# Optimization experiments

Measured on AMD Instinct MI355X. Metric: run time of the kernel, lower is better.

Reference implementation:

```python
import jax, jax.numpy as jnp
import numpy as np

B, S, D, H = 2, 2048, 1024, 16
DK = D // H
ROPE_BASE = 10000


def _rope_tables(seq_len, dim):
    # RotaryEmbedding.__call__: freqs [S, dim/2], emb = concat([freqs, freqs]) -> [S, dim]
    inv_freq = 1.0 / (ROPE_BASE ** (jnp.arange(0, dim, 2, dtype=jnp.float32) / dim))
    t = jnp.arange(seq_len, dtype=jnp.float32)
    freqs = jnp.outer(t, inv_freq)
    emb = jnp.concatenate([freqs, freqs], axis=-1)
    return jnp.cos(emb), jnp.sin(emb)


def _apply_rope(x, cos, sin):
    # Faithful to apply_rotary_pos_emb: interleaved even/odd channel rotation
    cos = cos[None, None, :, :]  # [1,1,S,DK]
    sin = sin[None, None, :, :]
    x1 = x[..., 0::2]
    x2 = x[..., 1::2]
    r1 = x1 * cos[..., 0::2] - x2 * sin[..., 1::2]
    r2 = x1 * sin[..., 0::2] + x2 * cos[..., 1::2]
    return jnp.stack([r1, r2], axis=-1).reshape(x.shape)


def setup_inputs() -> dict:
    key = jax.random.key(0)
    ks = jax.random.split(key, 11)
    xavier = lambda k: jax.random.uniform(k, (D, D), jnp.float32,
                                          -jnp.sqrt(6.0 / (D + D)), jnp.sqrt(6.0 / (D + D)))
    return {
        "query": jax.random.normal(ks[0], (B, S, D), jnp.float32),
        "key": jax.random.normal(ks[1], (B, S, D), jnp.float32),
        "value": jax.random.normal(ks[2], (B, S, D), jnp.float32),
        "Wq": xavier(ks[3]), "bq": jnp.zeros((D,), jnp.float32),
        "Wk": xavier(ks[4]), "bk": jnp.zeros((D,), jnp.float32),
        "Wv": xavier(ks[5]), "bv": jnp.zeros((D,), jnp.float32),
        "Wo": xavier(ks[6]), "bo": jnp.zeros((D,), jnp.float32),
    }


def reference(query, key, value, Wq, bq, Wk, bk, Wv, bv, Wo, bo):
    def split_heads(x):  # [B,S,D] -> [B,H,S,DK]
        return x.reshape(B, S, H, DK).transpose(0, 2, 1, 3)

    q = split_heads(query @ Wq + bq)
    k = split_heads(key @ Wk + bk)
    v = split_heads(value @ Wv + bv)

    cos, sin = _rope_tables(S, DK)
    q = _apply_rope(q, cos, sin)
    k = _apply_rope(k, cos, sin)

    scores = jnp.einsum("bhqd,bhkd->bhqk", q, k) / jnp.sqrt(jnp.float32(DK))
    causal = jnp.tril(jnp.ones((S, S), dtype=bool))
    scores = jnp.where(causal, scores, jnp.float32(-1e10))
    attn = jax.nn.softmax(scores, axis=-1)
    out = jnp.einsum("bhqk,bhkd->bhqd", attn, v)  # [B,H,S,DK]
    out = out.transpose(0, 2, 1, 3).reshape(B, S, D)
    return out @ Wo + bo
```

## Files before the change

### kernel.cpp

```cpp
#include <hip/hip_runtime.h>
#include <hip/hip_bf16.h>
#include <math.h>

#define B_ 2
#define S_ 2048
#define D_ 1024
#define H_ 16
#define DK_ 64

#define ROPE_C 0.4152410118609203f
#define LOG2E 1.4426950408889634f

typedef float f4 __attribute__((ext_vector_type(4)));
typedef short s8 __attribute__((ext_vector_type(8)));

__device__ __forceinline__ ushort f2b(float f) {
  union { float f; uint u; } v; v.f = f;
  uint u = v.u + 0x7fffu + ((v.u >> 16) & 1u);
  return (ushort)(u >> 16);
}

__device__ __forceinline__ float b2f(ushort u) {
  union { uint u; float f; } v; v.u = ((uint)u) << 16;
  return v.f;
}

__device__ __forceinline__ uint cvtpk(float a, float b) {
  uint r;
  asm("v_cvt_pk_bf16_f32 %0, %1, %2" : "=v"(r) : "v"(a), "v"(b));
  return r;
}

__device__ __forceinline__ void async16(const ushort* g, ushort* l) {
  __builtin_amdgcn_global_load_lds(
      (const __attribute__((address_space(1))) uint*)g,
      (__attribute__((address_space(3))) uint*)l, 16, 0, 0);
}

__global__ __launch_bounds__(256) void prep_all(
    const float* __restrict__ q_in, const float* __restrict__ k_in,
    const float* __restrict__ v_in,
    ushort* __restrict__ Xbq, ushort* __restrict__ Xbk, ushort* __restrict__ Xbv,
    const float* __restrict__ Wq, const float* __restrict__ Wk,
    const float* __restrict__ Wv, const float* __restrict__ Wo,
    ushort* __restrict__ Wtqkv, ushort* __restrict__ Wto) {
  __shared__ ushort T[64][65];
  const int bid = blockIdx.x, t = threadIdx.x;
  if (bid < 6144) {
    const int m = bid >> 11;
    const float* in = (m == 0) ? q_in : (m == 1) ? k_in : v_in;
    ushort* out = (m == 0) ? Xbq : (m == 1) ? Xbk : Xbv;
    int idx = ((bid & 2047) * 256 + t) * 8;
    float4 a = *(const float4*)&in[idx];
    float4 b = *(const float4*)&in[idx + 4];
    ushort tmp[8] = {f2b(a.x), f2b(a.y), f2b(a.z), f2b(a.w),
                     f2b(b.x), f2b(b.y), f2b(b.z), f2b(b.w)};
    *(uint4*)&out[idx] = *(uint4*)tmp;
  } else {
    const int tb = bid - 6144;
    const int m = tb >> 8;
    const float* W = (m == 0) ? Wq : (m == 1) ? Wk : (m == 2) ? Wv : Wo;
    ushort* Wt = (m == 3) ? Wto : Wtqkv + (size_t)m * 1024 * 1024;
    const int k0 = (tb & 15) * 64, n0 = ((tb >> 4) & 15) * 64;
    #pragma unroll
    for (int i = 0; i < 16; ++i) {
      int e = t + i * 256, r = e >> 6, c = e & 63;
      T[c][r] = f2b(W[(size_t)(k0 + r) * D_ + n0 + c]);
    }
    __syncthreads();
    #pragma unroll
    for (int i = 0; i < 16; ++i) {
      int e = t + i * 256, r = e >> 6, c = e & 63;
      Wt[(size_t)(n0 + r) * D_ + k0 + c] = T[r][c];
    }
  }
}

template <int MODE>
__global__ __launch_bounds__(256) void gemm_mfma(
    const ushort* __restrict__ A0, const ushort* __restrict__ A1,
    const ushort* __restrict__ A2, const ushort* __restrict__ Bt,
    const float* __restrict__ bb0, const float* __restrict__ bb1,
    const float* __restrict__ bb2,
    ushort* __restrict__ oq, ushort* __restrict__ ok, ushort* __restrict__ ov,
    float* __restrict__ oo) {
  __shared__ ushort SM[16384];
  ushort* Es = SM;

  const int t = threadIdx.x, w = t >> 6, l = t & 63;
  const int m0 = blockIdx.x * 128, n0 = blockIdx.y * 128;
  const int wm = (w >> 1) * 64, wn = (w & 1) * 64;
  const int lm = l & 15, q4 = (l >> 4) * 4;
  const int hb = l >> 4;

  const ushort* A;
  const float* bias;
  int mat = 0;
  if constexpr (MODE == 0) {
    mat = n0 >> 10;
    A = (mat == 0) ? A0 : (mat == 1) ? A1 : A2;
    bias = (mat == 0) ? bb0 : (mat == 1) ? bb1 : bb2;
  } else {
    A = A0; bias = bb0;
  }

  const int srow = w * 32 + (l >> 2);
  const int pb = l & 3;
  const int lb = pb ^ (srow & 3);
  const ushort* gA = A + (size_t)(m0 + srow) * D_ + lb * 8;
  const ushort* gB = Bt + (size_t)(n0 + srow) * D_ + lb * 8;

#define GSTAGE(bf, kk)                                   \
  {                                                      \
    ushort* lA = SM + (bf) * 4096 + w * 1024;            \
    ushort* lB = SM + 8192 + (bf) * 4096 + w * 1024;     \
    async16(gA + (kk), lA);                              \
    async16(gA + 16 * D_ + (kk), lA + 512);              \
    async16(gB + (kk), lB);                              \
    async16(gB + 16 * D_ + (kk), lB + 512);              \
  }

  f4 acc[4][4];
  #pragma unroll
  for (int i = 0; i < 4; ++i)
    #pragma unroll
    for (int j = 0; j < 4; ++j) acc[i][j] = (f4){0.f, 0.f, 0.f, 0.f};

  GSTAGE(0, 0);
  __syncthreads();

  for (int k0 = 0; k0 < D_; k0 += 32) {
    const int bf = (k0 >> 5) & 1;
    if (k0 + 32 < D_) GSTAGE(bf ^ 1, k0 + 32);
    const ushort* Asb = SM + bf * 4096;
    const ushort* Bsb = SM + 8192 + bf * 4096;
    s8 af[4], bfr[4];
    #pragma unroll
    for (int mt = 0; mt < 4; ++mt) {
      int ra = wm + mt * 16 + lm;
      af[mt] = *(const s8*)&Asb[ra * 32 + ((hb ^ (ra & 3)) << 3)];
    }
    #pragma unroll
    for (int nt = 0; nt < 4; ++nt) {
      int rb = wn + nt * 16 + lm;
      bfr[nt] = *(const s8*)&Bsb[rb * 32 + ((hb ^ (rb & 3)) << 3)];
    }
    __builtin_amdgcn_s_setprio(1);
    #pragma unroll
    for (int mt = 0; mt < 4; ++mt)
      #pragma unroll
      for (int nt = 0; nt < 4; ++nt)
        acc[mt][nt] = __builtin_amdgcn_mfma_f32_16x16x32_bf16(af[mt], bfr[nt], acc[mt][nt], 0, 0, 0);
    __builtin_amdgcn_s_setprio(0);
    __syncthreads();
  }

  if constexpr (MODE == 2) {
    #pragma unroll
    for (int nt = 0; nt < 4; ++nt) {
      int n = n0 + wn + nt * 16 + lm;
      float bv = bias[n];
      #pragma unroll
      for (int mt = 0; mt < 4; ++mt)
        #pragma unroll
        for (int r = 0; r < 4; ++r)
          oo[(size_t)(m0 + wm + mt * 16 + q4 + r) * D_ + n] = acc[mt][nt][r] + bv;
    }
  } else {
    ushort* dst = (mat == 0) ? oq : (mat == 1) ? ok : ov;
    const int nm0 = n0 & 1023;
    #pragma unroll
    for (int p = 0; p < 2; ++p) {
      if ((w >> 1) == p) {
        #pragma unroll
        for (int nt = 0; nt < 4; ++nt) {
          int col = wn + nt * 16 + lm;
          float bv = bias[nm0 + col];
          #pragma unroll
          for (int mt = 0; mt < 4; ++mt)
            #pragma unroll
            for (int r = 0; r < 4; ++r)
              Es[(mt * 16 + q4 + r) * 144 + col] = f2b(acc[mt][nt][r] + bv);
        }
      }
      __syncthreads();
      #pragma unroll
      for (int i = 0; i < 4; ++i) {
        int e = t + i * 256, row = e >> 4, ch = e & 15;
        *(uint4*)&dst[(size_t)(m0 + p * 64 + row) * D_ + nm0 + ch * 8] =
            *(const uint4*)&Es[row * 144 + ch * 8];
      }
      __syncthreads();
    }
  }
#undef GSTAGE
}

__global__ __launch_bounds__(256) void rope_pass(
    const ushort* __restrict__ qtmp, const ushort* __restrict__ ktmp,
    const ushort* __restrict__ vtmp,
    ushort* __restrict__ qfb, ushort* __restrict__ kfb,
    ushort* __restrict__ vtb) {
  __shared__ ushort T[64][72];
  const int t = threadIdx.x;
  const int bh = blockIdx.x, st = blockIdx.y;
  const int b = bh >> 4, h = bh & 15;
  const int s0 = st * 64;
  const int r = t >> 2, c0 = (t & 3) * 16;
  const int s = s0 + r;

  float cs[16], sn[16];
  const float pos = (float)s;
  #pragma unroll
  for (int j = 0; j < 16; ++j) {
    float invf = exp2f(-(float)((c0 + j) & 31) * ROPE_C);
    __sincosf(pos * invf, &sn[j], &cs[j]);
  }

  const size_t src = ((size_t)(b * S_ + s)) * D_ + h * 64 + c0;
  const size_t dstqk = ((size_t)bh * S_ + s) * DK_ + c0;

  #pragma unroll
  for (int tensor = 0; tensor < 2; ++tensor) {
    const ushort* in = tensor ? ktmp : qtmp;
    ushort* out = tensor ? kfb : qfb;
    const float scale = tensor ? 1.f : 0.18033688011112042f;
    uint4 raw0 = *(const uint4*)&in[src];
    uint4 raw1 = *(const uint4*)&in[src + 8];
    ushort xr[16];
    *(uint4*)&xr[0] = raw0;
    *(uint4*)&xr[8] = raw1;
    float x[16];
    #pragma unroll
    for (int j = 0; j < 16; ++j) x[j] = b2f(xr[j]);
    ushort o[16];
    #pragma unroll
    for (int j = 0; j < 16; j += 2) {
      float e = x[j] * cs[j] - x[j + 1] * sn[j + 1];
      float d = x[j] * sn[j] + x[j + 1] * cs[j + 1];
      o[j] = f2b(e * scale);
      o[j + 1] = f2b(d * scale);
    }
    *(uint4*)&out[dstqk] = *(const uint4*)&o[0];
    *(uint4*)&out[dstqk + 8] = *(const uint4*)&o[8];
  }

  {
    uint4 raw0 = *(const uint4*)&vtmp[src];
    uint4 raw1 = *(const uint4*)&vtmp[src + 8];
    ushort xr[16];
    *(uint4*)&xr[0] = raw0;
    *(uint4*)&xr[8] = raw1;
    #pragma unroll
    for (int j = 0; j < 16; ++j) T[c0 + j][r] = xr[j];
    __syncthreads();
    const size_t dstv = ((size_t)bh * DK_ + r) * S_ + s0 + c0;
    *(uint4*)&vtb[dstv] = *(const uint4*)&T[r][c0];
    *(uint4*)&vtb[dstv + 8] = *(const uint4*)&T[r][c0 + 8];
  }
}

__global__ __launch_bounds__(256, 4) void attn_mfma(const ushort* __restrict__ qf,
                                                    const ushort* __restrict__ kf,
                                                    const ushort* __restrict__ vtf,
                                                    ushort* __restrict__ ctx) {
  __shared__ ushort Ks[2][4096];
  __shared__ ushort Vs[2][4096];
  __shared__ ushort PsS[4096];

  const int t = threadIdx.x, w = t >> 6, l = t & 63;
  const int bh = blockIdx.x, qt = 31 - (int)blockIdx.y;
  const int i0 = qt * 64;
  const int lm = l & 15, hb = l >> 4, h8 = hb * 8, q4 = hb * 4, w16 = w * 16;
  const size_t base = (size_t)bh * S_ * DK_;
  const int b = bh >> 4, h = bh & 15;

  const int sr = l >> 3, pbk = l & 7;
  const int rA = w * 16 + sr, rB = rA + 8;
  const int swS = (pbk ^ sr) << 3;
  const ushort* gkA = kf + base + (size_t)rA * DK_ + swS;
  const ushort* gkB = kf + base + (size_t)rB * DK_ + swS;
  const ushort* gvA = vtf + base + (size_t)rA * S_ + swS;
  const ushort* gvB = vtf + base + (size_t)rB * S_ + swS;

#define STAGE(bf, j0)                                       \
  {                                                         \
    ushort* lk = &Ks[bf][w * 1024];                         \
    ushort* lv = &Vs[bf][w * 1024];                         \
    async16(gkA + (size_t)(j0) * DK_, lk);                  \
    async16(gkB + (size_t)(j0) * DK_, lk + 512);            \
    async16(gvA + (j0), lv);                                \
    async16(gvB + (j0), lv + 512);                          \
  }

  const ushort* qp = qf + base + (size_t)(i0 + w16 + lm) * DK_ + h8;
  const s8 bq0 = *(const s8*)qp;
  const s8 bq1 = *(const s8*)(qp + 32);

  const int swr = lm & 7;
  const int cA = (hb ^ swr) << 3;
  const int cB = ((hb + 4) ^ swr) << 3;
  const int prow = (w16 + lm) * 64;
  const int psub = ((hb & 1) << 2) + ((hb >> 1) ^ swr);

  STAGE(0, 0);

  f4 O[4];
  #pragma unroll
  for (int i = 0; i < 4; ++i) O[i] = (f4){0.f, 0.f, 0.f, 0.f};
  float m_ = -1e30f, l_ = 0.f;

  __syncthreads();

  for (int jt = 0; jt <= qt; ++jt) {
    const int cur = jt & 1;
    if (jt < qt) STAGE(cur ^ 1, (jt + 1) * 64);
    const ushort* Kb = Ks[cur];
    const ushort* Vb = Vs[cur];

    f4 st[4];
    __builtin_amdgcn_s_setprio(1);
    #pragma unroll
    for (int nt = 0; nt < 4; ++nt) {
      const ushort* kRow = Kb + (nt * 16 + lm) * 64;
      s8 a0 = *(const s8*)&kRow[cA];
      s8 a1 = *(const s8*)&kRow[cB];
      f4 a = (f4){0.f, 0.f, 0.f, 0.f};
      a = __builtin_amdgcn_mfma_f32_16x16x32_bf16(a0, bq0, a, 0, 0, 0);
      a = __builtin_amdgcn_mfma_f32_16x16x32_bf16(a1, bq1, a, 0, 0, 0);
      st[nt] = a;
    }
    __builtin_amdgcn_s_setprio(0);

    if (jt == qt) {
      #pragma unroll
      for (int nt = 0; nt < 4; ++nt)
        #pragma unroll
        for (int r = 0; r < 4; ++r)
          if (nt * 16 + q4 + r > w16 + lm) st[nt][r] = -1e30f;
    }

    float x0 = fmaxf(fmaxf(st[0][0], st[0][1]), fmaxf(st[0][2], st[0][3]));
    float x1 = fmaxf(fmaxf(st[1][0], st[1][1]), fmaxf(st[1][2], st[1][3]));
    float x2 = fmaxf(fmaxf(st[2][0], st[2][1]), fmaxf(st[2][2], st[2][3]));
    float x3 = fmaxf(fmaxf(st[3][0], st[3][1]), fmaxf(st[3][2], st[3][3]));
    float pm = fmaxf(fmaxf(x0, x1), fmaxf(x2, x3));
    pm = fmaxf(pm, __shfl_xor(pm, 16));
    pm = fmaxf(pm, __shfl_xor(pm, 32));

    const bool stable = __all(pm <= m_ + 4.0f);
    float mn = m_, alpha = 1.f;
    if (!stable) {
      mn = fmaxf(m_, pm);
      alpha = exp2f(m_ - mn);
      m_ = mn;
    }

    #pragma unroll
    for (int nt = 0; nt < 4; ++nt)
      #pragma unroll
      for (int r = 0; r < 4; ++r)
        st[nt][r] = exp2f(st[nt][r] - mn);
    float s0 = (st[0][0] + st[0][1]) + (st[0][2] + st[0][3]);
    float s1 = (st[1][0] + st[1][1]) + (st[1][2] + st[1][3]);
    float s2 = (st[2][0] + st[2][1]) + (st[2][2] + st[2][3]);
    float s3 = (st[3][0] + st[3][1]) + (st[3][2] + st[3][3]);
    float ps = (s0 + s1) + (s2 + s3);
    ps += __shfl_xor(ps, 16);
    ps += __shfl_xor(ps, 32);

    if (stable) {
      l_ += ps;
    } else {
      l_ = l_ * alpha + ps;
      float ar[4];
      #pragma unroll
      for (int r = 0; r < 4; ++r) ar[r] = __shfl(alpha, q4 + r);
      #pragma unroll
      for (int nt = 0; nt < 4; ++nt)
        #pragma unroll
        for (int r = 0; r < 4; ++r) O[nt][r] *= ar[r];
    }

    #pragma unroll
    for (int nt = 0; nt < 4; ++nt) {
      uint2 pp;
      pp.x = cvtpk(st[nt][0], st[nt][1]);
      pp.y = cvtpk(st[nt][2], st[nt][3]);
      const int pidx = prow + ((((nt << 1) + (hb >> 1)) ^ swr) << 3) + ((hb & 1) << 2);
      *(uint2*)&PsS[pidx] = pp;
    }
    s8 ap0 = *(const s8*)&PsS[prow + cA];
    s8 ap1 = *(const s8*)&PsS[prow + cB];

    __builtin_amdgcn_s_setprio(1);
    #pragma unroll
    for (int nt = 0; nt < 4; ++nt) {
      const ushort* vRow = Vb + (nt * 16 + lm) * 64;
      s8 v0 = *(const s8*)&vRow[cA];
      s8 v1 = *(const s8*)&vRow[cB];
      O[nt] = __builtin_amdgcn_mfma_f32_16x16x32_bf16(ap0, v0, O[nt], 0, 0, 0);
      O[nt] = __builtin_amdgcn_mfma_f32_16x16x32_bf16(ap1, v1, O[nt], 0, 0, 0);
    }
    __builtin_amdgcn_s_setprio(0);

    __syncthreads();
  }

  float il[4];
  #pragma unroll
  for (int r = 0; r < 4; ++r) il[r] = 1.f / __shfl(l_, q4 + r);
  #pragma unroll
  for (int nt = 0; nt < 4; ++nt)
    #pragma unroll
    for (int r = 0; r < 4; ++r) {
      int row = w16 + q4 + r, col = nt * 16 + lm;
      PsS[row * 64 + ((((col >> 3) ^ (row & 7)) << 3)) + (col & 7)] =
          f2b(O[nt][r] * il[r]);
    }
  __syncthreads();
  #pragma unroll
  for (int i = 0; i < 2; ++i) {
    int e = t + i * 256, row = e >> 3, ch = e & 7;
    int s = i0 + row;
    *(uint4*)&ctx[((size_t)(b * S_ + s)) * D_ + h * 64 + ch * 8] =
        *(const uint4*)&PsS[row * 64 + ((ch ^ (row & 7)) << 3)];
  }
#undef STAGE
}

extern "C" void kernel_launch(void* const* d_in, const int* in_sizes, int n_in,
                              void* d_out, int out_size, void* d_ws, size_t ws_size,
                              hipStream_t stream) {
  const float* q_in = (const float*)d_in[0];
  const float* k_in = (const float*)d_in[1];
  const float* v_in = (const float*)d_in[2];
  const float* Wq = (const float*)d_in[3];
  const float* bq = (const float*)d_in[4];
  const float* Wk = (const float*)d_in[5];
  const float* bk = (const float*)d_in[6];
  const float* Wv = (const float*)d_in[7];
  const float* bv = (const float*)d_in[8];
  const float* Wo = (const float*)d_in[9];
  const float* bo = (const float*)d_in[10];

  const size_t NE = (size_t)B_ * S_ * D_;
  ushort* Xbq = (ushort*)d_ws;
  ushort* Xbk = Xbq + NE;
  ushort* Xbv = Xbk + NE;
  ushort* Wtqkv = Xbv + NE;
  ushort* Wto = Wtqkv + 3 * 1024 * 1024;
  ushort* qtmp = Wto + 1024 * 1024;
  ushort* ktmp = qtmp + NE;
  ushort* vtmp = ktmp + NE;
  ushort* qfb = vtmp + NE;
  ushort* kfb = qfb + NE;
  ushort* vtb = kfb + NE;
  ushort* ctxb = qtmp;

  prep_all<<<7168, 256, 0, stream>>>(q_in, k_in, v_in, Xbq, Xbk, Xbv,
                                     Wq, Wk, Wv, Wo, Wtqkv, Wto);

  gemm_mfma<0><<<dim3(32, 24), 256, 0, stream>>>(
      Xbq, Xbk, Xbv, Wtqkv, bq, bk, bv, qtmp, ktmp, vtmp, nullptr);

  rope_pass<<<dim3(32, 32), 256, 0, stream>>>(qtmp, ktmp, vtmp, qfb, kfb, vtb);

  attn_mfma<<<dim3(32, 32), 256, 0, stream>>>(qfb, kfb, vtb, ctxb);

  gemm_mfma<2><<<dim3(32, 8), 256, 0, stream>>>(
      ctxb, ctxb, ctxb, Wto, bo, bo, bo, nullptr, nullptr, nullptr,
      (float*)d_out);
}
```

Baseline: 228.7 us.

## Switch attention to 32x32x16 MFMA with two waves and register-shuffled P

After: 238.6 us. 1.04x slower.

```diff
diff --git a/kernel.cpp b/kernel.cpp
--- a/kernel.cpp
+++ b/kernel.cpp
@@ -12,6 +12,7 @@
 #define LOG2E 1.4426950408889634f
 
 typedef float f4 __attribute__((ext_vector_type(4)));
+typedef float f16x __attribute__((ext_vector_type(16)));
 typedef short s8 __attribute__((ext_vector_type(8)));
 
 __device__ __forceinline__ ushort f2b(float f) {
@@ -260,54 +261,49 @@
   }
 }
 
-__global__ __launch_bounds__(256, 4) void attn_mfma(const ushort* __restrict__ qf,
+__global__ __launch_bounds__(128, 2) void attn_mfma(const ushort* __restrict__ qf,
                                                     const ushort* __restrict__ kf,
                                                     const ushort* __restrict__ vtf,
                                                     ushort* __restrict__ ctx) {
   __shared__ ushort Ks[2][4096];
   __shared__ ushort Vs[2][4096];
-  __shared__ ushort PsS[4096];
 
   const int t = threadIdx.x, w = t >> 6, l = t & 63;
   const int bh = blockIdx.x, qt = 31 - (int)blockIdx.y;
   const int i0 = qt * 64;
-  const int lm = l & 15, hb = l >> 4, h8 = hb * 8, q4 = hb * 4, w16 = w * 16;
+  const int lo = l & 31, hi = l >> 5;
   const size_t base = (size_t)bh * S_ * DK_;
   const int b = bh >> 4, h = bh & 15;
 
   const int sr = l >> 3, pbk = l & 7;
-  const int rA = w * 16 + sr, rB = rA + 8;
   const int swS = (pbk ^ sr) << 3;
-  const ushort* gkA = kf + base + (size_t)rA * DK_ + swS;
-  const ushort* gkB = kf + base + (size_t)rB * DK_ + swS;
-  const ushort* gvA = vtf + base + (size_t)rA * S_ + swS;
-  const ushort* gvB = vtf + base + (size_t)rB * S_ + swS;
-
-#define STAGE(bf, j0)                                       \
-  {                                                         \
-    ushort* lk = &Ks[bf][w * 1024];                         \
-    ushort* lv = &Vs[bf][w * 1024];                         \
-    async16(gkA + (size_t)(j0) * DK_, lk);                  \
-    async16(gkB + (size_t)(j0) * DK_, lk + 512);            \
-    async16(gvA + (j0), lv);                                \
-    async16(gvB + (j0), lv + 512);                          \
-  }
-
-  const ushort* qp = qf + base + (size_t)(i0 + w16 + lm) * DK_ + h8;
-  const s8 bq0 = *(const s8*)qp;
-  const s8 bq1 = *(const s8*)(qp + 32);
-
-  const int swr = lm & 7;
-  const int cA = (hb ^ swr) << 3;
-  const int cB = ((hb + 4) ^ swr) << 3;
-  const int prow = (w16 + lm) * 64;
-  const int psub = ((hb & 1) << 2) + ((hb >> 1) ^ swr);
+  const ushort* gk = kf + base + (size_t)sr * DK_ + swS;
+  const ushort* gv = vtf + base + (size_t)sr * S_ + swS;
+
+#define STAGE(bf, j0)                                                      \
+  if (w == 0) {                                                            \
+    _Pragma("unroll")                                                      \
+    for (int i = 0; i < 8; ++i)                                            \
+      async16(gk + (size_t)((j0) + 8 * i) * DK_, &Ks[bf][i * 512]);        \
+  } else {                                                                 \
+    _Pragma("unroll")                                                      \
+    for (int i = 0; i < 8; ++i)                                            \
+      async16(gv + (size_t)(8 * i) * S_ + (j0), &Vs[bf][i * 512]);         \
+  }
+
+  const ushort* qp = qf + base + (size_t)(i0 + w * 32 + lo) * DK_;
+  s8 bq[4];
+  #pragma unroll
+  for (int s = 0; s < 4; ++s) bq[s] = *(const s8*)&qp[s * 16 + hi * 8];
+
+  const int rsw = lo & 7;
+  const int roff = lo * 64;
 
   STAGE(0, 0);
 
-  f4 O[4];
+  f16x O0, O1;
   #pragma unroll
-  for (int i = 0; i < 4; ++i) O[i] = (f4){0.f, 0.f, 0.f, 0.f};
+  for (int r = 0; r < 16; ++r) { O0[r] = 0.f; O1[r] = 0.f; }
   float m_ = -1e30f, l_ = 0.f;
 
   __syncthreads();
@@ -318,113 +314,128 @@
     const ushort* Kb = Ks[cur];
     const ushort* Vb = Vs[cur];
 
-    f4 st[4];
+    f16x s0, s1;
+    #pragma unroll
+    for (int r = 0; r < 16; ++r) { s0[r] = 0.f; s1[r] = 0.f; }
     __builtin_amdgcn_s_setprio(1);
     #pragma unroll
-    for (int nt = 0; nt < 4; ++nt) {
-      const ushort* kRow = Kb + (nt * 16 + lm) * 64;
-      s8 a0 = *(const s8*)&kRow[cA];
-      s8 a1 = *(const s8*)&kRow[cB];
-      f4 a = (f4){0.f, 0.f, 0.f, 0.f};
-      a = __builtin_amdgcn_mfma_f32_16x16x32_bf16(a0, bq0, a, 0, 0, 0);
-      a = __builtin_amdgcn_mfma_f32_16x16x32_bf16(a1, bq1, a, 0, 0, 0);
-      st[nt] = a;
+    for (int s = 0; s < 4; ++s) {
+      const int co = ((2 * s + hi) ^ rsw) << 3;
+      s8 a0 = *(const s8*)&Kb[roff + co];
+      s8 a1 = *(const s8*)&Kb[2048 + roff + co];
+      s0 = __builtin_amdgcn_mfma_f32_32x32x16_bf16(a0, bq[s], s0, 0, 0, 0);
+      s1 = __builtin_amdgcn_mfma_f32_32x32x16_bf16(a1, bq[s], s1, 0, 0, 0);
     }
     __builtin_amdgcn_s_setprio(0);
 
     if (jt == qt) {
-      #pragma unroll
-      for (int nt = 0; nt < 4; ++nt)
-        #pragma unroll
-        for (int r = 0; r < 4; ++r)
-          if (nt * 16 + q4 + r > w16 + lm) st[nt][r] = -1e30f;
-    }
-
-    float x0 = fmaxf(fmaxf(st[0][0], st[0][1]), fmaxf(st[0][2], st[0][3]));
-    float x1 = fmaxf(fmaxf(st[1][0], st[1][1]), fmaxf(st[1][2], st[1][3]));
-    float x2 = fmaxf(fmaxf(st[2][0], st[2][1]), fmaxf(st[2][2], st[2][3]));
-    float x3 = fmaxf(fmaxf(st[3][0], st[3][1]), fmaxf(st[3][2], st[3][3]));
-    float pm = fmaxf(fmaxf(x0, x1), fmaxf(x2, x3));
-    pm = fmaxf(pm, __shfl_xor(pm, 16));
+      const int qr = 32 * w + lo;
+      #pragma unroll
+      for (int r = 0; r < 16; ++r) {
+        const int kb0 = 8 * (r >> 2) + 4 * hi + (r & 3);
+        if (kb0 > qr) s0[r] = -1e30f;
+        if (kb0 + 32 > qr) s1[r] = -1e30f;
+      }
+    }
+
+    float pm = s0[0];
+    #pragma unroll
+    for (int r = 1; r < 16; ++r) pm = fmaxf(pm, s0[r]);
+    #pragma unroll
+    for (int r = 0; r < 16; ++r) pm = fmaxf(pm, s1[r]);
     pm = fmaxf(pm, __shfl_xor(pm, 32));
 
     const bool stable = __all(pm <= m_ + 4.0f);
-    float mn = m_, alpha = 1.f;
-    if (!stable) {
-      mn = fmaxf(m_, pm);
-      alpha = exp2f(m_ - mn);
-      m_ = mn;
-    }
-
-    #pragma unroll
-    for (int nt = 0; nt < 4; ++nt)
-      #pragma unroll
-      for (int r = 0; r < 4; ++r)
-        st[nt][r] = exp2f(st[nt][r] - mn);
-    float s0 = (st[0][0] + st[0][1]) + (st[0][2] + st[0][3]);
-    float s1 = (st[1][0] + st[1][1]) + (st[1][2] + st[1][3]);
-    float s2 = (st[2][0] + st[2][1]) + (st[2][2] + st[2][3]);
-    float s3 = (st[3][0] + st[3][1]) + (st[3][2] + st[3][3]);
-    float ps = (s0 + s1) + (s2 + s3);
-    ps += __shfl_xor(ps, 16);
+    float mn = m_;
+    if (!stable) mn = fmaxf(m_, pm);
+
+    #pragma unroll
+    for (int r = 0; r < 16; ++r) {
+      s0[r] = exp2f(s0[r] - mn);
+      s1[r] = exp2f(s1[r] - mn);
+    }
+    float ps = s0[0];
+    #pragma unroll
+    for (int r = 1; r < 16; ++r) ps += s0[r];
+    #pragma unroll
+    for (int r = 0; r < 16; ++r) ps += s1[r];
     ps += __shfl_xor(ps, 32);
 
     if (stable) {
       l_ += ps;
     } else {
+      const float alpha = exp2f(m_ - mn);
+      m_ = mn;
       l_ = l_ * alpha + ps;
-      float ar[4];
-      #pragma unroll
-      for (int r = 0; r < 4; ++r) ar[r] = __shfl(alpha, q4 + r);
-      #pragma unroll
-      for (int nt = 0; nt < 4; ++nt)
-        #pragma unroll
-        for (int r = 0; r < 4; ++r) O[nt][r] *= ar[r];
-    }
-
-    #pragma unroll
-    for (int nt = 0; nt < 4; ++nt) {
-      uint2 pp;
-      pp.x = cvtpk(st[nt][0], st[nt][1]);
-      pp.y = cvtpk(st[nt][2], st[nt][3]);
-      const int pidx = prow + ((((nt << 1) + (hb >> 1)) ^ swr) << 3) + ((hb & 1) << 2);
-      *(uint2*)&PsS[pidx] = pp;
-    }
-    s8 ap0 = *(const s8*)&PsS[prow + cA];
-    s8 ap1 = *(const s8*)&PsS[prow + cB];
+      #pragma unroll
+      for (int r = 0; r < 16; ++r) { O0[r] *= alpha; O1[r] *= alpha; }
+    }
+
+    uint pk0[8], pk1[8];
+    #pragma unroll
+    for (int m = 0; m < 8; ++m) {
+      pk0[m] = cvtpk(s0[2 * m], s0[2 * m + 1]);
+      pk1[m] = cvtpk(s1[2 * m], s1[2 * m + 1]);
+    }
+    uint zz0[4], zz1[4];
+    {
+      uint z0[4], z1[4];
+      z0[0] = hi ? pk0[0] : pk0[2];  z0[1] = hi ? pk0[1] : pk0[3];
+      z0[2] = hi ? pk0[4] : pk0[6];  z0[3] = hi ? pk0[5] : pk0[7];
+      z1[0] = hi ? pk1[0] : pk1[2];  z1[1] = hi ? pk1[1] : pk1[3];
+      z1[2] = hi ? pk1[4] : pk1[6];  z1[3] = hi ? pk1[5] : pk1[7];
+      #pragma unroll
+      for (int c = 0; c < 4; ++c) {
+        zz0[c] = __shfl_xor((int)z0[c], 32);
+        zz1[c] = __shfl_xor((int)z1[c], 32);
+      }
+    }
+    uint bw[16];
+    bw[0]  = hi ? zz0[0] : pk0[0];  bw[1]  = hi ? zz0[1] : pk0[1];
+    bw[2]  = hi ? pk0[2] : zz0[0];  bw[3]  = hi ? pk0[3] : zz0[1];
+    bw[4]  = hi ? zz0[2] : pk0[4];  bw[5]  = hi ? zz0[3] : pk0[5];
+    bw[6]  = hi ? pk0[6] : zz0[2];  bw[7]  = hi ? pk0[7] : zz0[3];
+    bw[8]  = hi ? zz1[0] : pk1[0];  bw[9]  = hi ? zz1[1] : pk1[1];
+    bw[10] = hi ? pk1[2] : zz1[0];  bw[11] = hi ? pk1[3] : zz1[1];
+    bw[12] = hi ? zz1[2] : pk1[4];  bw[13] = hi ? zz1[3] : pk1[5];
+    bw[14] = hi ? pk1[6] : zz1[2];  bw[15] = hi ? pk1[7] : zz1[3];
+    const s8* bfr = (const s8*)bw;
 
     __builtin_amdgcn_s_setprio(1);
     #pragma unroll
-    for (int nt = 0; nt < 4; ++nt) {
-      const ushort* vRow = Vb + (nt * 16 + lm) * 64;
-      s8 v0 = *(const s8*)&vRow[cA];
-      s8 v1 = *(const s8*)&vRow[cB];
-      O[nt] = __builtin_amdgcn_mfma_f32_16x16x32_bf16(ap0, v0, O[nt], 0, 0, 0);
-      O[nt] = __builtin_amdgcn_mfma_f32_16x16x32_bf16(ap1, v1, O[nt], 0, 0, 0);
+    for (int s = 0; s < 4; ++s) {
+      const int co = ((2 * s + hi) ^ rsw) << 3;
+      s8 a0 = *(const s8*)&Vb[roff + co];
+      s8 a1 = *(const s8*)&Vb[2048 + roff + co];
+      O0 = __builtin_amdgcn_mfma_f32_32x32x16_bf16(a0, bfr[s], O0, 0, 0, 0);
+      O1 = __builtin_amdgcn_mfma_f32_32x32x16_bf16(a1, bfr[s], O1, 0, 0, 0);
     }
     __builtin_amdgcn_s_setprio(0);
 
     __syncthreads();
   }
 
-  float il[4];
-  #pragma unroll
-  for (int r = 0; r < 4; ++r) il[r] = 1.f / __shfl(l_, q4 + r);
-  #pragma unroll
-  for (int nt = 0; nt < 4; ++nt)
-    #pragma unroll
-    for (int r = 0; r < 4; ++r) {
-      int row = w16 + q4 + r, col = nt * 16 + lm;
-      PsS[row * 64 + ((((col >> 3) ^ (row & 7)) << 3)) + (col & 7)] =
-          f2b(O[nt][r] * il[r]);
-    }
-  __syncthreads();
-  #pragma unroll
-  for (int i = 0; i < 2; ++i) {
-    int e = t + i * 256, row = e >> 3, ch = e & 7;
-    int s = i0 + row;
-    *(uint4*)&ctx[((size_t)(b * S_ + s)) * D_ + h * 64 + ch * 8] =
-        *(const uint4*)&PsS[row * 64 + ((ch ^ (row & 7)) << 3)];
+  {
+    const float il = 1.f / l_;
+    ushort* Ts = &Ks[0][0];
+    const int q = w * 32 + lo;
+    #pragma unroll
+    for (int r = 0; r < 16; r += 2) {
+      const int o = r >> 2;
+      const int sub = (4 * hi + (r & 3)) * 2;
+      uint v0 = cvtpk(O0[r] * il, O0[r + 1] * il);
+      uint v1 = cvtpk(O1[r] * il, O1[r + 1] * il);
+      *(uint*)((char*)Ts + q * 128 + ((o ^ (q & 7)) << 4) + sub) = v0;
+      *(uint*)((char*)Ts + q * 128 + (((4 + o) ^ (q & 7)) << 4) + sub) = v1;
+    }
+    __syncthreads();
+    #pragma unroll
+    for (int i = 0; i < 4; ++i) {
+      int e = t + i * 128, row = e >> 3, ch = e & 7;
+      int sg = i0 + row;
+      *(uint4*)&ctx[((size_t)(b * S_ + sg)) * D_ + h * 64 + ch * 8] =
+          *(const uint4*)((const char*)Ts + row * 128 + ((ch ^ (row & 7)) << 4));
+    }
   }
 #undef STAGE
 }
@@ -466,7 +477,7 @@
 
   rope_pass<<<dim3(32, 32), 256, 0, stream>>>(qtmp, ktmp, vtmp, qfb, kfb, vtb);
 
-  attn_mfma<<<dim3(32, 32), 256, 0, stream>>>(qfb, kfb, vtb, ctxb);
+  attn_mfma<<<dim3(32, 32), 128, 0, stream>>>(qfb, kfb, vtb, ctxb);
 
   gemm_mfma<2><<<dim3(32, 8), 256, 0, stream>>>(
       ctxb, ctxb, ctxb, Wto, bo, bo, bo, nullptr, nullptr, nullptr,
```

## Fuse RoPE, Q scaling and V transpose into QKV GEMM epilogue

Applied to the files above, without the earlier changes.

Measured after the change: 218.3 us. -4.6%, faster.

```diff
diff --git a/kernel.cpp b/kernel.cpp
--- a/kernel.cpp
+++ b/kernel.cpp
@@ -10,6 +10,7 @@
 
 #define ROPE_C 0.4152410118609203f
 #define LOG2E 1.4426950408889634f
+#define QSCALE 0.18033688011112042f
 
 typedef float f4 __attribute__((ext_vector_type(4)));
 typedef short s8 __attribute__((ext_vector_type(8)));
@@ -167,97 +168,89 @@
           oo[(size_t)(m0 + wm + mt * 16 + q4 + r) * D_ + n] = acc[mt][nt][r] + bv;
     }
   } else {
-    ushort* dst = (mat == 0) ? oq : (mat == 1) ? ok : ov;
     const int nm0 = n0 & 1023;
-    #pragma unroll
-    for (int p = 0; p < 2; ++p) {
-      if ((w >> 1) == p) {
+    const int bI = m0 >> 11;
+    if (mat < 2) {
+      ushort* dst = (mat == 0) ? oq : ok;
+      const float scale = (mat == 0) ? QSCALE : 1.f;
+      #pragma unroll
+      for (int p = 0; p < 2; ++p) {
+        if ((w >> 1) == p) {
+          #pragma unroll
+          for (int nt = 0; nt < 4; ++nt) {
+            int col = wn + nt * 16 + lm;
+            float bv = bias[nm0 + col];
+            #pragma unroll
+            for (int mt = 0; mt < 4; ++mt)
+              #pragma unroll
+              for (int r = 0; r < 4; ++r)
+                Es[(mt * 16 + q4 + r) * 144 + col] = f2b(acc[mt][nt][r] + bv);
+          }
+        }
+        __syncthreads();
         #pragma unroll
-        for (int nt = 0; nt < 4; ++nt) {
-          int col = wn + nt * 16 + lm;
-          float bv = bias[nm0 + col];
+        for (int i = 0; i < 4; ++i) {
+          int e = t + i * 256, row = e >> 4, ch = e & 15;
+          int sg = m0 + p * 64 + row;
+          int s = sg & 2047;
+          int dcol = nm0 + ch * 8;
+          int hh = dcol >> 6, dk0 = dcol & 63;
+          ushort xr[8];
+          *(uint4*)xr = *(const uint4*)&Es[row * 144 + ch * 8];
+          float x[8];
           #pragma unroll
-          for (int mt = 0; mt < 4; ++mt)
+          for (int j = 0; j < 8; ++j) x[j] = b2f(xr[j]);
+          const float pos = (float)s;
+          ushort o[8];
+          #pragma unroll
+          for (int j = 0; j < 8; j += 2) {
+            int dg = dk0 + j;
+            float inve = exp2f(-(float)(dg & 31) * ROPE_C);
+            float invo = exp2f(-(float)((dg + 1) & 31) * ROPE_C);
+            float se, ce, so, co;
+            __sincosf(pos * inve, &se, &ce);
+            __sincosf(pos * invo, &so, &co);
+            float ev = x[j] * ce - x[j + 1] * so;
+            float od = x[j] * se + x[j + 1] * co;
+            o[j] = f2b(ev * scale);
+            o[j + 1] = f2b(od * scale);
+          }
+          size_t didx = ((size_t)((bI * 16 + hh) * S_ + s)) * DK_ + dk0;
+          *(uint4*)&dst[didx] = *(const uint4*)o;
+        }
+        __syncthreads();
+      }
+    } else {
+      #pragma unroll
+      for (int p = 0; p < 2; ++p) {
+        if ((w >> 1) == p) {
+          #pragma unroll
+          for (int nt = 0; nt < 4; ++nt) {
+            int col = wn + nt * 16 + lm;
+            float bv = bias[nm0 + col];
             #pragma unroll
-            for (int r = 0; r < 4; ++r)
-              Es[(mt * 16 + q4 + r) * 144 + col] = f2b(acc[mt][nt][r] + bv);
+            for (int mt = 0; mt < 4; ++mt)
+              #pragma unroll
+              for (int r = 0; r < 4; ++r)
+                Es[col * 72 + (mt * 16 + q4 + r)] = f2b(acc[mt][nt][r] + bv);
+          }
         }
+        __syncthreads();
+        #pragma unroll
+        for (int i = 0; i < 4; ++i) {
+          int e = t + i * 256, d = e >> 3, sc = e & 7;
+          int dcol = nm0 + d;
+          int hh = dcol >> 6, dkv = dcol & 63;
+          int sg = m0 + p * 64 + sc * 8;
+          int s = sg & 2047;
+          size_t didx = ((size_t)((bI * 16 + hh) * DK_ + dkv)) * S_ + s;
+          *(uint4*)&ov[didx] = *(const uint4*)&Es[d * 72 + sc * 8];
+        }
+        __syncthreads();
       }
-      __syncthreads();
-      #pragma unroll
-      for (int i = 0; i < 4; ++i) {
-        int e = t + i * 256, row = e >> 4, ch = e & 15;
-        *(uint4*)&dst[(size_t)(m0 + p * 64 + row) * D_ + nm0 + ch * 8] =
-            *(const uint4*)&Es[row * 144 + ch * 8];
-      }
-      __syncthreads();
     }
   }
 #undef GSTAGE
-}
-
-__global__ __launch_bounds__(256) void rope_pass(
-    const ushort* __restrict__ qtmp, const ushort* __restrict__ ktmp,
-    const ushort* __restrict__ vtmp,
-    ushort* __restrict__ qfb, ushort* __restrict__ kfb,
-    ushort* __restrict__ vtb) {
-  __shared__ ushort T[64][72];
-  const int t = threadIdx.x;
-  const int bh = blockIdx.x, st = blockIdx.y;
-  const int b = bh >> 4, h = bh & 15;
-  const int s0 = st * 64;
-  const int r = t >> 2, c0 = (t & 3) * 16;
-  const int s = s0 + r;
-
-  float cs[16], sn[16];
-  const float pos = (float)s;
-  #pragma unroll
-  for (int j = 0; j < 16; ++j) {
-    float invf = exp2f(-(float)((c0 + j) & 31) * ROPE_C);
-    __sincosf(pos * invf, &sn[j], &cs[j]);
-  }
-
-  const size_t src = ((size_t)(b * S_ + s)) * D_ + h * 64 + c0;
-  const size_t dstqk = ((size_t)bh * S_ + s) * DK_ + c0;
-
-  #pragma unroll
-  for (int tensor = 0; tensor < 2; ++tensor) {
-    const ushort* in = tensor ? ktmp : qtmp;
-    ushort* out = tensor ? kfb : qfb;
-    const float scale = tensor ? 1.f : 0.18033688011112042f;
-    uint4 raw0 = *(const uint4*)&in[src];
-    uint4 raw1 = *(const uint4*)&in[src + 8];
-    ushort xr[16];
-    *(uint4*)&xr[0] = raw0;
-    *(uint4*)&xr[8] = raw1;
-    float x[16];
-    #pragma unroll
-    for (int j = 0; j < 16; ++j) x[j] = b2f(xr[j]);
-    ushort o[16];
-    #pragma unroll
-    for (int j = 0; j < 16; j += 2) {
-      float e = x[j] * cs[j] - x[j + 1] * sn[j + 1];
-      float d = x[j] * sn[j] + x[j + 1] * cs[j + 1];
-      o[j] = f2b(e * scale);
-      o[j + 1] = f2b(d * scale);
-    }
-    *(uint4*)&out[dstqk] = *(const uint4*)&o[0];
-    *(uint4*)&out[dstqk + 8] = *(const uint4*)&o[8];
-  }
-
-  {
-    uint4 raw0 = *(const uint4*)&vtmp[src];
-    uint4 raw1 = *(const uint4*)&vtmp[src + 8];
-    ushort xr[16];
-    *(uint4*)&xr[0] = raw0;
-    *(uint4*)&xr[8] = raw1;
-    #pragma unroll
-    for (int j = 0; j < 16; ++j) T[c0 + j][r] = xr[j];
-    __syncthreads();
-    const size_t dstv = ((size_t)bh * DK_ + r) * S_ + s0 + c0;
-    *(uint4*)&vtb[dstv] = *(const uint4*)&T[r][c0];
-    *(uint4*)&vtb[dstv + 8] = *(const uint4*)&T[r][c0 + 8];
-  }
 }
 
 __global__ __launch_bounds__(256, 4) void attn_mfma(const ushort* __restrict__ qf,
@@ -276,12 +269,11 @@
   const int b = bh >> 4, h = bh & 15;
 
   const int sr = l >> 3, pbk = l & 7;
-  const int rA = w * 16 + sr, rB = rA + 8;
   const int swS = (pbk ^ sr) << 3;
-  const ushort* gkA = kf + base + (size_t)rA * DK_ + swS;
-  const ushort* gkB = kf + base + (size_t)rB * DK_ + swS;
-  const ushort* gvA = vtf + base + (size_t)rA * S_ + swS;
-  const ushort* gvB = vtf + base + (size_t)rB * S_ + swS;
+  const ushort* gkA = kf + base + (size_t)(w * 16 + sr) * DK_ + swS;
+  const ushort* gkB = kf + base + (size_t)(w * 16 + sr + 8) * DK_ + swS;
+  const ushort* gvA = vtf + base + (size_t)(w * 16 + sr) * S_ + swS;
+  const ushort* gvB = vtf + base + (size_t)(w * 16 + sr + 8) * S_ + swS;
 
 #define STAGE(bf, j0)                                       \
   {                                                         \
@@ -301,7 +293,6 @@
   const int cA = (hb ^ swr) << 3;
   const int cB = ((hb + 4) ^ swr) << 3;
   const int prow = (w16 + lm) * 64;
-  const int psub = ((hb & 1) << 2) + ((hb >> 1) ^ swr);
 
   STAGE(0, 0);
 
@@ -450,21 +441,16 @@
   ushort* Xbv = Xbk + NE;
   ushort* Wtqkv = Xbv + NE;
   ushort* Wto = Wtqkv + 3 * 1024 * 1024;
-  ushort* qtmp = Wto + 1024 * 1024;
-  ushort* ktmp = qtmp + NE;
-  ushort* vtmp = ktmp + NE;
-  ushort* qfb = vtmp + NE;
+  ushort* qfb = Wto + 1024 * 1024;
   ushort* kfb = qfb + NE;
   ushort* vtb = kfb + NE;
-  ushort* ctxb = qtmp;
+  ushort* ctxb = vtb + NE;
 
   prep_all<<<7168, 256, 0, stream>>>(q_in, k_in, v_in, Xbq, Xbk, Xbv,
                                      Wq, Wk, Wv, Wo, Wtqkv, Wto);
 
   gemm_mfma<0><<<dim3(32, 24), 256, 0, stream>>>(
-      Xbq, Xbk, Xbv, Wtqkv, bq, bk, bv, qtmp, ktmp, vtmp, nullptr);
-
-  rope_pass<<<dim3(32, 32), 256, 0, stream>>>(qtmp, ktmp, vtmp, qfb, kfb, vtb);
+      Xbq, Xbk, Xbv, Wtqkv, bq, bk, bv, qfb, kfb, vtb, nullptr);
 
   attn_mfma<<<dim3(32, 32), 256, 0, stream>>>(qfb, kfb, vtb, ctxb);
 
```
